# Performance work log

Hardware: AMD Instinct MI355X
Metric: run time of the kernel (lower is better)

## Reference

```python
import jax, jax.numpy as jnp
import numpy as np

N, H, V = 8192, 1024, 32000
IGNORE_INDEX = -100
LABEL_SMOOTHING = 0.0
LOGIT_SCALE = 1.0


def setup_inputs() -> dict:
    key = jax.random.key(0)
    k1, k2, k3 = jax.random.split(key, 3)
    x = jax.random.normal(k1, (N, H), dtype=jnp.float32)
    weight = jax.random.normal(k2, (V, H), dtype=jnp.float32) * 0.02
    bias = jnp.zeros((V,), dtype=jnp.float32)
    target = jax.random.randint(k3, (N,), 0, V, dtype=jnp.int64)
    return {"x": x, "weight": weight, "bias": bias, "target": target}


def reference(x, weight, bias, target):
    # logits: [N, V]; fused kernel never materializes this fully, but math is identical
    logits = (x @ weight.T + bias) * LOGIT_SCALE
    lse = jax.nn.logsumexp(logits.astype(jnp.float32), axis=-1)  # [N]
    valid = target != IGNORE_INDEX
    safe_t = jnp.where(valid, target, 0)
    tgt_logit = jnp.take_along_axis(logits, safe_t[:, None], axis=-1)[:, 0]
    loss_i = lse - tgt_logit
    if LABEL_SMOOTHING > 0:
        eps = LABEL_SMOOTHING / V
        z = (-eps * logits).sum(-1)
        loss_i = loss_i * (1.0 - LABEL_SMOOTHING) + (z + LABEL_SMOOTHING * lse)
    loss_i = jnp.where(valid, loss_i, 0.0)
    total = jnp.maximum(valid.sum(), 1)
    # reduction == 'mean': each per-token loss divided by total, then summed
    return loss_i.sum() / total
```

## Files before the change

kernel.cpp:

```cpp
#include <hip/hip_runtime.h>
#include <math.h>

typedef int    intx8    __attribute__((ext_vector_type(8)));
typedef float  floatx16 __attribute__((ext_vector_type(16)));

#define N_ROWS 8192
#define H_DIM  1024
#define V_DIM  32000
#define V_PAD  32768
#define IGNORE_INDEX (-100)

#define S_SPLITS 16
#define TILES_PER_SPLIT 16
#define BM 256
#define BN 128
#define KSTEPS 16
#define TOTAL_STEPS (TILES_PER_SPLIT * KSTEPS)
#define BBUF (4 * 128 * 16)

#define LOG2E 1.4426950408889634f
#define LN2   0.6931471805599453f

__global__ __launch_bounds__(256) void convert_fp8(const float* __restrict__ in,
                                                   unsigned char* __restrict__ out,
                                                   int Rstride, float scale) {
  const int r = blockIdx.x * 256 + threadIdx.x;
  const int u = blockIdx.y;
  const float4* src = (const float4*)(in + (size_t)r * H_DIM + u * 16);
  uint4 res;
#pragma unroll
  for (int j = 0; j < 4; ++j) {
    const float4 v = src[j];
    int p = __builtin_amdgcn_cvt_pk_fp8_f32(v.x * scale, v.y * scale, 0, false);
    p = __builtin_amdgcn_cvt_pk_fp8_f32(v.z * scale, v.w * scale, p, true);
    ((int*)&res)[j] = p;
  }
  *(uint4*)(out + ((size_t)u * Rstride + r) * 16) = res;
}

__global__ __launch_bounds__(256) void pad_bias(const float* __restrict__ bias,
                                                float* __restrict__ biasp) {
  const int i = blockIdx.x * 256 + threadIdx.x;
  biasp[i] = (i < V_DIM) ? bias[i] * LOG2E : -1e30f;
}


typedef union { intx8 v; uint4 q[2]; } afrag;

#define BDMA(T) do {                                                                     \
    const int _t = (T);                                                                  \
    const int _ub = (_t & 15) * 4;                                                       \
    const int _n0 = (sidx * TILES_PER_SPLIT + (_t >> 4)) * BN;                           \
    unsigned char* _d = smB + ((_t & 1) ? BBUF : 0);                                     \
    _Pragma("unroll")                                                                    \
    for (int _j = 0; _j < 2; ++_j) {                                                     \
      const int _c = _j * 4 + w, _u = _c >> 1, _rb = _c & 1;                             \
      __builtin_amdgcn_global_load_lds(                                                  \
          (const __attribute__((address_space(1))) void*)(wsb +                          \
              ((size_t)(_ub + _u) * V_PAD + _n0 + _rb * 64 + lane) * 16),                \
          (__attribute__((address_space(3))) void*)(_d + ((_u * 128 + _rb * 64 + lane) * 16)), \
          16, 0, 0);                                                                     \
    }                                                                                    \
  } while (0)

#define ALD(T, DST) do {                                                                 \
    const int _u2 = ((T) & 15) * 4 + half * 2;                                           \
    DST[0].q[0] = *(const uint4*)(xs + (((size_t)(_u2    ) * N_ROWS + arow0) * 16));     \
    DST[0].q[1] = *(const uint4*)(xs + (((size_t)(_u2 + 1) * N_ROWS + arow0) * 16));     \
    DST[1].q[0] = *(const uint4*)(xs + (((size_t)(_u2    ) * N_ROWS + arow1) * 16));     \
    DST[1].q[1] = *(const uint4*)(xs + (((size_t)(_u2 + 1) * N_ROWS + arow1) * 16));     \
  } while (0)

#define STEP(T, AU, AL) do {                                                             \
    const int _st = (T);                                                                 \
    __syncthreads();       \
    if (_st + 1 < TOTAL_STEPS) {                                                         \
      BDMA(_st + 1);                                                                     \
      ALD(_st + 1, AL);                                                                  \
    }                                                                                    \
    const unsigned char* _pB = smB + ((_st & 1) ? BBUF : 0);                             \
    afrag b[4];                                                                          \
    const int _ua = half * 2;                                                            \
    _Pragma("unroll")                                                                    \
    for (int nb = 0; nb < 4; ++nb) {                                                     \
      b[nb].q[0] = *(const uint4*)(_pB + ((_ua * 128 + nb * 32 + l31) * 16));            \
      b[nb].q[1] = *(const uint4*)(_pB + (((_ua + 1) * 128 + nb * 32 + l31) * 16));      \
    }                                                                                    \
    __builtin_amdgcn_s_setprio(1);                                                       \
    _Pragma("unroll")                                                                    \
    for (int mb = 0; mb < 2; ++mb)                                                       \
      _Pragma("unroll")                                                                  \
      for (int nb = 0; nb < 4; ++nb)                                                     \
        acc[mb][nb] = __builtin_amdgcn_mfma_scale_f32_32x32x64_f8f6f4(                   \
            AU[mb].v, b[nb].v, acc[mb][nb],                                              \
            0, 0,                                                  \
            0, 0x7F7F7F7F,                                            \
            0, 0x7F7F7F7F);                                           \
    __builtin_amdgcn_s_setprio(0);                                                       \
  } while (0)

__global__ __launch_bounds__(256, 2) void flce_main(const unsigned char* __restrict__ xs,
                                                    const unsigned char* __restrict__ wsb,
                                                    const float* __restrict__ biasp,
                                                    float* __restrict__ partials) {
  __shared__ __align__(16) unsigned char smB[2 * BBUF];

  const int tid  = threadIdx.x;
  const int lane = tid & 63;
  const int w    = tid >> 6;
  const int l31  = lane & 31;
  const int half = lane >> 5;
  const int wr   = w * 64;

  const int hw     = blockIdx.y * 32 + blockIdx.x;
  const int rowblk = hw >> 4;
  const int sidx   = ((hw & 7) << 1) | ((hw >> 3) & 1);
  const int row0   = rowblk * BM;

  const size_t arow0 = (size_t)(row0 + wr + l31);
  const size_t arow1 = arow0 + 32;

  float l_state[32];
#pragma unroll
  for (int i = 0; i < 32; ++i) l_state[i] = 0.f;

  afrag aE[2], aO[2];

  BDMA(0);
  ALD(0, aE);

#pragma unroll 1
  for (int ct = 0; ct < TILES_PER_SPLIT; ++ct) {
    floatx16 acc[2][4];
#pragma unroll
    for (int mb = 0; mb < 2; ++mb)
#pragma unroll
      for (int nb = 0; nb < 4; ++nb)
#pragma unroll
        for (int i = 0; i < 16; ++i) acc[mb][nb][i] = 0.f;

#pragma unroll 1
    for (int ks2 = 0; ks2 < 8; ++ks2) {
      const int st0 = ct * KSTEPS + ks2 * 2;
      STEP(st0,     aE, aO);
      STEP(st0 + 1, aO, aE);
    }

    const int n0 = (sidx * TILES_PER_SPLIT + ct) * BN;
    float bnb[4];
#pragma unroll
    for (int nb = 0; nb < 4; ++nb) bnb[nb] = biasp[n0 + nb * 32 + l31];
#pragma unroll
    for (int mb = 0; mb < 2; ++mb)
#pragma unroll
      for (int r = 0; r < 16; ++r) {
        float s = exp2f(acc[mb][0][r] + bnb[0]) + exp2f(acc[mb][1][r] + bnb[1])
                + exp2f(acc[mb][2][r] + bnb[2]) + exp2f(acc[mb][3][r] + bnb[3]);
        l_state[mb * 16 + r] += s;
      }
  }

#pragma unroll
  for (int s = 0; s < 32; ++s) {
    float v = l_state[s];
#pragma unroll
    for (int off = 1; off < 32; off <<= 1) v += __shfl_xor(v, off, 64);
    l_state[s] = v;
  }

  if (l31 == 0) {
#pragma unroll
    for (int s = 0; s < 32; ++s) {
      const int mb = s >> 4, r = s & 15;
      const int row = wr + mb * 32 + 4 * half + (r & 3) + 8 * (r >> 2);
      partials[(size_t)(row0 + row) * S_SPLITS + sidx] = l_state[s];
    }
  }
}

__global__ __launch_bounds__(256) void tgt_kernel(const float* __restrict__ x,
                                                  const float* __restrict__ wgt,
                                                  const float* __restrict__ bias,
                                                  const int* __restrict__ target,
                                                  float* __restrict__ tgt_logit) {
  const int r = blockIdx.x * 4 + (threadIdx.x >> 6);
  const int lane = threadIdx.x & 63;
  const int t = target[r];
  const int tt = (t == IGNORE_INDEX) ? 0 : t;
  const float4* xr = (const float4*)(x + (size_t)r * H_DIM);
  const float4* wr = (const float4*)(wgt + (size_t)tt * H_DIM);
  float acc = 0.f;
#pragma unroll
  for (int i = 0; i < 4; ++i) {
    const float4 a = xr[lane + i * 64];
    const float4 b = wr[lane + i * 64];
    acc += a.x * b.x + a.y * b.y + a.z * b.z + a.w * b.w;
  }
#pragma unroll
  for (int off = 32; off >= 1; off >>= 1) acc += __shfl_xor(acc, off, 64);
  if (lane == 0) tgt_logit[r] = acc + bias[tt];
}

__global__ __launch_bounds__(256) void loss_rows(const float* __restrict__ partials,
                                                 const float* __restrict__ tgt_logit,
                                                 const int* __restrict__ target,
                                                 float* __restrict__ bsums) {
  const int r = blockIdx.x * 256 + threadIdx.x;
  float l = 0.f;
#pragma unroll
  for (int s = 0; s < S_SPLITS; ++s) l += partials[(size_t)r * S_SPLITS + s];
  const float lse = LN2 * __log2f(l);
  const bool valid = (target[r] != IGNORE_INDEX);
  float loss = valid ? (lse - tgt_logit[r]) : 0.f;
  float cnt  = valid ? 1.f : 0.f;
  const int lane = threadIdx.x & 63;
  const int w = threadIdx.x >> 6;
#pragma unroll
  for (int off = 32; off >= 1; off >>= 1) {
    loss += __shfl_xor(loss, off, 64);
    cnt  += __shfl_xor(cnt, off, 64);
  }
  __shared__ float sl[4], sc[4];
  if (lane == 0) { sl[w] = loss; sc[w] = cnt; }
  __syncthreads();
  if (threadIdx.x == 0) {
    float S = 0.f, C = 0.f;
    for (int i = 0; i < 4; ++i) { S += sl[i]; C += sc[i]; }
    bsums[blockIdx.x] = S;
    bsums[32 + blockIdx.x] = C;
  }
}

__global__ void finalize(const float* __restrict__ bsums, float* __restrict__ out) {
  const int t = threadIdx.x;
  float s = (t < 32) ? bsums[t] : 0.f;
  float c = (t < 32) ? bsums[32 + t] : 0.f;
#pragma unroll
  for (int off = 32; off >= 1; off >>= 1) {
    s += __shfl_xor(s, off, 64);
    c += __shfl_xor(c, off, 64);
  }
  if (t == 0) out[0] = s / fmaxf(c, 1.f);
}

extern "C" void kernel_launch(void* const* d_in, const int* in_sizes, int n_in,
                              void* d_out, int out_size, void* d_ws, size_t ws_size,
                              hipStream_t stream) {
  const float* x    = (const float*)d_in[0];
  const float* wgt  = (const float*)d_in[1];
  const float* bias = (const float*)d_in[2];
  const int*   tgt  = (const int*)d_in[3];
  float* out = (float*)d_out;

  char* ws = (char*)d_ws;
  const size_t XS8 = (size_t)N_ROWS * H_DIM;
  const size_t WS8 = (size_t)V_PAD * H_DIM;
  const size_t BP  = (size_t)V_PAD * 4;
  const size_t PB  = (size_t)N_ROWS * S_SPLITS * 4;
  unsigned char* xs8 = (unsigned char*)ws;
  unsigned char* ws8 = (unsigned char*)(ws + XS8);
  float* biasp    = (float*)(ws + XS8 + WS8);
  float* partials = (float*)(ws + XS8 + WS8 + BP);
  float* tgt_lg   = (float*)(ws + XS8 + WS8 + BP + PB);
  float* bsums    = (float*)(ws + XS8 + WS8 + BP + PB + (size_t)N_ROWS * 4);

  convert_fp8<<<dim3(N_ROWS / 256, H_DIM / 16), 256, 0, stream>>>(x, xs8, N_ROWS, LOG2E);
  convert_fp8<<<dim3(V_DIM / 256, H_DIM / 16), 256, 0, stream>>>(wgt, ws8, V_PAD, 1.0f);
  pad_bias<<<V_PAD / 256, 256, 0, stream>>>(bias, biasp);
  tgt_kernel<<<N_ROWS / 4, 256, 0, stream>>>(x, wgt, bias, tgt, tgt_lg);
  flce_main<<<dim3(N_ROWS / BM, S_SPLITS), 256, 0, stream>>>(xs8, ws8, biasp, partials);
  loss_rows<<<N_ROWS / 256, 256, 0, stream>>>(partials, tgt_lg, tgt, bsums);
  finalize<<<1, 64, 0, stream>>>(bsums, out);
}
```

Before: 555.0 us.

## Halve row tile to 128, double K chunk per step, raise occupancy

```diff
diff --git a/kernel.cpp b/kernel.cpp
--- a/kernel.cpp
+++ b/kernel.cpp
@@ -12,11 +12,11 @@
 
 #define S_SPLITS 16
 #define TILES_PER_SPLIT 16
-#define BM 256
+#define BM 128
 #define BN 128
-#define KSTEPS 16
+#define KSTEPS 8
 #define TOTAL_STEPS (TILES_PER_SPLIT * KSTEPS)
-#define BBUF (4 * 128 * 16)
+#define BBUF (8 * 128 * 16)
 
 #define LOG2E 1.4426950408889634f
 #define LN2   0.6931471805599453f
@@ -45,15 +45,15 @@
 }
 
 
-typedef union { intx8 v; uint4 q[2]; } afrag;
+typedef union { intx8 v; uint4 q[2]; } frag;
 
 #define BDMA(T) do {                                                                     \
     const int _t = (T);                                                                  \
-    const int _ub = (_t & 15) * 4;                                                       \
-    const int _n0 = (sidx * TILES_PER_SPLIT + (_t >> 4)) * BN;                           \
+    const int _ub = (_t & 7) * 8;                                                        \
+    const int _n0 = (sidx * TILES_PER_SPLIT + (_t >> 3)) * BN;                           \
     unsigned char* _d = smB + ((_t & 1) ? BBUF : 0);                                     \
     _Pragma("unroll")                                                                    \
-    for (int _j = 0; _j < 2; ++_j) {                                                     \
+    for (int _j = 0; _j < 4; ++_j) {                                                     \
       const int _c = _j * 4 + w, _u = _c >> 1, _rb = _c & 1;                             \
       __builtin_amdgcn_global_load_lds(                                                  \
           (const __attribute__((address_space(1))) void*)(wsb +                          \
@@ -63,43 +63,49 @@
     }                                                                                    \
   } while (0)
 
-#define ALD(T, DST) do {                                                                 \
-    const int _u2 = ((T) & 15) * 4 + half * 2;                                           \
-    DST[0].q[0] = *(const uint4*)(xs + (((size_t)(_u2    ) * N_ROWS + arow0) * 16));     \
-    DST[0].q[1] = *(const uint4*)(xs + (((size_t)(_u2 + 1) * N_ROWS + arow0) * 16));     \
-    DST[1].q[0] = *(const uint4*)(xs + (((size_t)(_u2    ) * N_ROWS + arow1) * 16));     \
-    DST[1].q[1] = *(const uint4*)(xs + (((size_t)(_u2 + 1) * N_ROWS + arow1) * 16));     \
-  } while (0)
-
-#define STEP(T, AU, AL) do {                                                             \
+#define STEP(T, AK0, AK0N) do {                                                          \
     const int _st = (T);                                                                 \
-    __syncthreads();       \
+    __syncthreads();                \
+    if (_st + 1 < TOTAL_STEPS) BDMA(_st + 1);                                            \
+    frag aK1;                   \
+    {                                                                                    \
+      const size_t _u1 = (size_t)((_st & 7) * 8 + 4 + half2);                            \
+      aK1.q[0] = *(const uint4*)(xs + ((_u1 * N_ROWS + arow) * 16));                     \
+      aK1.q[1] = *(const uint4*)(xs + (((_u1 + 1) * N_ROWS + arow) * 16));               \
+    }                                                                                    \
     if (_st + 1 < TOTAL_STEPS) {                                                         \
-      BDMA(_st + 1);                                                                     \
-      ALD(_st + 1, AL);                                                                  \
+      const size_t _u0 = (size_t)(((_st + 1) & 7) * 8 + half2);                          \
+      AK0N.q[0] = *(const uint4*)(xs + ((_u0 * N_ROWS + arow) * 16));                    \
+      AK0N.q[1] = *(const uint4*)(xs + (((_u0 + 1) * N_ROWS + arow) * 16));              \
     }                                                                                    \
     const unsigned char* _pB = smB + ((_st & 1) ? BBUF : 0);                             \
-    afrag b[4];                                                                          \
-    const int _ua = half * 2;                                                            \
+    frag b0[4];                                                                          \
     _Pragma("unroll")                                                                    \
     for (int nb = 0; nb < 4; ++nb) {                                                     \
-      b[nb].q[0] = *(const uint4*)(_pB + ((_ua * 128 + nb * 32 + l31) * 16));            \
-      b[nb].q[1] = *(const uint4*)(_pB + (((_ua + 1) * 128 + nb * 32 + l31) * 16));      \
+      b0[nb].q[0] = *(const uint4*)(_pB + (((half2    ) * 128 + nb * 32 + l31) * 16));   \
+      b0[nb].q[1] = *(const uint4*)(_pB + (((half2 + 1) * 128 + nb * 32 + l31) * 16));   \
     }                                                                                    \
     __builtin_amdgcn_s_setprio(1);                                                       \
     _Pragma("unroll")                                                                    \
-    for (int mb = 0; mb < 2; ++mb)                                                       \
-      _Pragma("unroll")                                                                  \
-      for (int nb = 0; nb < 4; ++nb)                                                     \
-        acc[mb][nb] = __builtin_amdgcn_mfma_scale_f32_32x32x64_f8f6f4(                   \
-            AU[mb].v, b[nb].v, acc[mb][nb],                                              \
-            0, 0,                                                  \
-            0, 0x7F7F7F7F,                                            \
-            0, 0x7F7F7F7F);                                           \
+    for (int nb = 0; nb < 4; ++nb)                                                       \
+      acc[nb] = __builtin_amdgcn_mfma_scale_f32_32x32x64_f8f6f4(                         \
+          AK0.v, b0[nb].v, acc[nb], 0, 0, 0, 0x7F7F7F7F, 0, 0x7F7F7F7F);                 \
+    __builtin_amdgcn_s_setprio(0);                                                       \
+    frag b1[4];                                                                          \
+    _Pragma("unroll")                                                                    \
+    for (int nb = 0; nb < 4; ++nb) {                                                     \
+      b1[nb].q[0] = *(const uint4*)(_pB + (((4 + half2) * 128 + nb * 32 + l31) * 16));   \
+      b1[nb].q[1] = *(const uint4*)(_pB + (((5 + half2) * 128 + nb * 32 + l31) * 16));   \
+    }                                                                                    \
+    __builtin_amdgcn_s_setprio(1);                                                       \
+    _Pragma("unroll")                                                                    \
+    for (int nb = 0; nb < 4; ++nb)                                                       \
+      acc[nb] = __builtin_amdgcn_mfma_scale_f32_32x32x64_f8f6f4(                         \
+          aK1.v, b1[nb].v, acc[nb], 0, 0, 0, 0x7F7F7F7F, 0, 0x7F7F7F7F);                 \
     __builtin_amdgcn_s_setprio(0);                                                       \
   } while (0)
 
-__global__ __launch_bounds__(256, 2) void flce_main(const unsigned char* __restrict__ xs,
+__global__ __launch_bounds__(256, 3) void flce_main(const unsigned char* __restrict__ xs,
                                                     const unsigned char* __restrict__ wsb,
                                                     const float* __restrict__ biasp,
                                                     float* __restrict__ partials) {
@@ -110,37 +116,35 @@
   const int w    = tid >> 6;
   const int l31  = lane & 31;
   const int half = lane >> 5;
-  const int wr   = w * 64;
-
-  const int hw     = blockIdx.y * 32 + blockIdx.x;
-  const int rowblk = hw >> 4;
-  const int sidx   = ((hw & 7) << 1) | ((hw >> 3) & 1);
-  const int row0   = rowblk * BM;
-
-  const size_t arow0 = (size_t)(row0 + wr + l31);
-  const size_t arow1 = arow0 + 32;
-
-  float l_state[32];
-#pragma unroll
-  for (int i = 0; i < 32; ++i) l_state[i] = 0.f;
-
-  afrag aE[2], aO[2];
+  const int half2 = half * 2;
+  const int row0 = blockIdx.x * BM;
+  const int sidx = blockIdx.y;
+
+  const size_t arow = (size_t)(row0 + w * 32 + l31);
+
+  float l_state[16];
+#pragma unroll
+  for (int i = 0; i < 16; ++i) l_state[i] = 0.f;
+
+  frag aE, aO;
 
   BDMA(0);
-  ALD(0, aE);
+  {
+    const size_t _u0 = (size_t)half2;
+    aE.q[0] = *(const uint4*)(xs + ((_u0 * N_ROWS + arow) * 16));
+    aE.q[1] = *(const uint4*)(xs + (((_u0 + 1) * N_ROWS + arow) * 16));
+  }
 
 #pragma unroll 1
   for (int ct = 0; ct < TILES_PER_SPLIT; ++ct) {
-    floatx16 acc[2][4];
-#pragma unroll
-    for (int mb = 0; mb < 2; ++mb)
-#pragma unroll
-      for (int nb = 0; nb < 4; ++nb)
-#pragma unroll
-        for (int i = 0; i < 16; ++i) acc[mb][nb][i] = 0.f;
+    floatx16 acc[4];
+#pragma unroll
+    for (int nb = 0; nb < 4; ++nb)
+#pragma unroll
+      for (int i = 0; i < 16; ++i) acc[nb][i] = 0.f;
 
 #pragma unroll 1
-    for (int ks2 = 0; ks2 < 8; ++ks2) {
+    for (int ks2 = 0; ks2 < 4; ++ks2) {
       const int st0 = ct * KSTEPS + ks2 * 2;
       STEP(st0,     aE, aO);
       STEP(st0 + 1, aO, aE);
@@ -151,17 +155,15 @@
 #pragma unroll
     for (int nb = 0; nb < 4; ++nb) bnb[nb] = biasp[n0 + nb * 32 + l31];
 #pragma unroll
-    for (int mb = 0; mb < 2; ++mb)
-#pragma unroll
-      for (int r = 0; r < 16; ++r) {
-        float s = exp2f(acc[mb][0][r] + bnb[0]) + exp2f(acc[mb][1][r] + bnb[1])
-                + exp2f(acc[mb][2][r] + bnb[2]) + exp2f(acc[mb][3][r] + bnb[3]);
-        l_state[mb * 16 + r] += s;
-      }
-  }
-
-#pragma unroll
-  for (int s = 0; s < 32; ++s) {
+    for (int r = 0; r < 16; ++r) {
+      float s = exp2f(acc[0][r] + bnb[0]) + exp2f(acc[1][r] + bnb[1])
+              + exp2f(acc[2][r] + bnb[2]) + exp2f(acc[3][r] + bnb[3]);
+      l_state[r] += s;
+    }
+  }
+
+#pragma unroll
+  for (int s = 0; s < 16; ++s) {
     float v = l_state[s];
 #pragma unroll
     for (int off = 1; off < 32; off <<= 1) v += __shfl_xor(v, off, 64);
@@ -170,9 +172,8 @@
 
   if (l31 == 0) {
 #pragma unroll
-    for (int s = 0; s < 32; ++s) {
-      const int mb = s >> 4, r = s & 15;
-      const int row = wr + mb * 32 + 4 * half + (r & 3) + 8 * (r >> 2);
+    for (int s = 0; s < 16; ++s) {
+      const int row = w * 32 + 4 * half + (s & 3) + 8 * (s >> 2);
       partials[(size_t)(row0 + row) * S_SPLITS + sidx] = l_state[s];
     }
   }
```

Result: slower. 1.474 ms (+165.6%).
